# Kernel tuning notes

Hardware: AMD Instinct MI355X
Metric: run time of the kernel (lower is better)

## Reference

```python
import jax, jax.numpy as jnp
import numpy as np

D_STATE = 64
HEADDIM = 64
KD = 4

def _layernorm(x, w, b, eps=1e-5):
    m = jnp.mean(x, axis=-1, keepdims=True)
    v = jnp.mean((x - m) ** 2, axis=-1, keepdims=True)
    return (x - m) / jnp.sqrt(v + eps) * w + b

def _adaptive_pool_matrix(n_in, n_out):
    # torch AdaptiveAvgPool2d bin edges: [floor(i*n/o), ceil((i+1)*n/o))
    P = np.zeros((n_out, n_in), np.float32)
    for i in range(n_out):
        s = (i * n_in) // n_out
        e = -((-(i + 1) * n_in) // n_out)
        P[i, s:e] = 1.0 / (e - s)
    return jnp.asarray(P)

def _vss(x, i, vln_w, vln_b, vin_w, vin_b, vconv_w, vconv_b, vxproj_w, vdt_bias, vA_log, vD, von_w, von_b, vout_w, vout_b):
    # VSSBlock (m0_noz): x + SS2D(LayerNorm(x)); x: (Bt, H, W, C) channels-last
    xn = _layernorm(x, vln_w[i], vln_b[i])
    u = xn @ vin_w[i].T + vin_b[i]                      # (Bt,H,W,Din) in_proj (no z branch)
    Bt, H, W, Din = u.shape
    v = jnp.transpose(u, (0, 3, 1, 2))
    v = jax.lax.conv_general_dilated(v, vconv_w[i][:, None], (1, 1), [(1, 1), (1, 1)],
                                     feature_group_count=Din,
                                     dimension_numbers=('NCHW', 'OIHW', 'NCHW'))
    v = v + vconv_b[i][None, :, None, None]
    v = jax.nn.gelu(jnp.transpose(v, (0, 2, 3, 1)))     # depthwise 3x3 + act
    L = H * W
    NH = Din // HEADDIM
    x_row = v.reshape(Bt, L, Din)
    x_col = jnp.transpose(v, (0, 2, 1, 3)).reshape(Bt, L, Din)
    xs = jnp.stack([x_row, x_col, x_row[:, ::-1], x_col[:, ::-1]], 1)  # cross-scan (Bt,KD,L,Din)
    x_dbl = jnp.einsum('bkld,kcd->bklc', xs, vxproj_w[i])              # dt | B | C
    dts = jax.nn.softplus(x_dbl[..., :NH] + vdt_bias[i][None, :, None, :])  # (Bt,KD,L,NH)
    Bm = x_dbl[..., NH:NH + D_STATE]
    Cm = x_dbl[..., NH + D_STATE:]
    A = -jnp.exp(vA_log[i])                             # (KD,NH) scalar-per-head (mamba2)
    xh = xs.reshape(Bt, KD, L, NH, HEADDIM)
    def step(h, t):
        dt_t, x_t, B_t, C_t = t                         # (Bt,KD,NH),(Bt,KD,NH,hd),(Bt,KD,N),(Bt,KD,N)
        dA = jnp.exp(dt_t * A)
        h = h * dA[..., None, None] + (dt_t[..., None] * x_t)[..., None] * B_t[:, :, None, None, :]
        y = jnp.einsum('bkhdn,bkn->bkhd', h, C_t)
        return h, y
    h0 = jnp.zeros((Bt, KD, NH, HEADDIM, D_STATE), x.dtype)
    seq = (jnp.moveaxis(dts, 2, 0), jnp.moveaxis(xh, 2, 0), jnp.moveaxis(Bm, 2, 0), jnp.moveaxis(Cm, 2, 0))
    _, ys = jax.lax.scan(step, h0, seq)                 # (L,Bt,KD,NH,hd)
    ys = jnp.moveaxis(ys, 0, 2) + vD[i][None, :, None, :, None] * xh   # D skip per head
    ys = ys.reshape(Bt, KD, L, Din)
    def uncol(t):
        return jnp.transpose(t.reshape(Bt, W, H, Din), (0, 2, 1, 3)).reshape(Bt, L, Din)
    y = ys[:, 0] + uncol(ys[:, 1]) + ys[:, 2, ::-1] + uncol(ys[:, 3, ::-1])  # cross-merge
    y = _layernorm(y, von_w[i], von_b[i])
    out = y.reshape(Bt, H, W, Din) @ vout_w[i].T + vout_b[i]
    return x + out

def reference(style, mask, content, pos_embed_c, pos_embed_s, newps_w, newps_b,
              vln_w, vln_b, vin_w, vin_b, vconv_w, vconv_b, vxproj_w, vdt_bias, vA_log, vD,
              von_w, von_b, vout_w, vout_b, lin1_w, lin1_b, lin2_w, lin2_b,
              dn1_w, dn1_b, dn2_w, dn2_b, dn3_w, dn3_b, decnorm_w, decnorm_b):
    # mask and the incoming pos_embed_c are unused, matching the torch forward
    B, C, H, W = content.shape
    Ph = _adaptive_pool_matrix(H, 18)
    Pw = _adaptive_pool_matrix(W, 18)
    pooled = jnp.einsum('ih,bchw,jw->bcij', Ph, content, Pw)            # AdaptiveAvgPool2d(18)
    pos_c = jnp.einsum('oc,bcij->boij', newps_w, pooled) + newps_b[None, :, None, None]
    pos_c = jax.image.resize(pos_c, (B, C, style.shape[2], style.shape[3]), method='linear')
    def to_seq(t):  # (B,C,H,W) -> (HW, B, 1, C)
        return jnp.transpose(t.reshape(t.shape[0], t.shape[1], -1), (2, 0, 1))[:, :, None, :]
    s = to_seq(style); c = to_seq(content); ps = to_seq(pos_embed_s); pc = to_seq(pos_c)
    vss = lambda x, i: _vss(x, i, vln_w, vln_b, vin_w, vin_b, vconv_w, vconv_b, vxproj_w,
                            vdt_bias, vA_log, vD, von_w, von_b, vout_w, vout_b)
    s_enc = vss(s, 0)
    c_enc = vss(c, 1)
    q = c_enc + pc
    k = s_enc + ps
    tgt = _layernorm(c_enc + vss(q, 2), dn1_w, dn1_b)
    tgt = tgt + _layernorm(s_enc + vss(k, 3), dn2_w, dn2_b)
    ffn = jax.nn.gelu(tgt @ lin1_w.T + lin1_b) @ lin2_w.T + lin2_b
    tgt = _layernorm(tgt + ffn, dn3_w, dn3_b)
    tgt = _layernorm(tgt, decnorm_w, decnorm_b)
    hs = jnp.transpose(tgt[:, :, 0, :], (1, 2, 0))                      # (B,C,L)
    Hq = int(np.sqrt(hs.shape[-1]))
    return hs.reshape(B, C, -1, Hq)

def setup_inputs():
    key = jax.random.key(0)
    ks = jax.random.split(key, 16)
    D = 512; DIN = 512; NH = DIN // HEADDIM; NB = 4
    f = lambda k, shape, s=0.02: jax.random.normal(k, shape, jnp.float32) * s
    return {
        'style': jax.random.normal(ks[0], (4, 512, 16, 16), jnp.float32),
        'mask': jnp.zeros((4, 256), jnp.bool_),
        'content': jax.random.normal(ks[1], (4, 512, 16, 16), jnp.float32),
        'pos_embed_c': jax.random.normal(ks[2], (4, 512, 16, 16), jnp.float32),
        'pos_embed_s': jax.random.normal(ks[3], (4, 512, 16, 16), jnp.float32),
        'newps_w': f(ks[4], (512, 512)), 'newps_b': jnp.zeros((512,), jnp.float32),
        'vln_w': jnp.ones((NB, D), jnp.float32), 'vln_b': jnp.zeros((NB, D), jnp.float32),
        'vin_w': f(ks[5], (NB, DIN, D)), 'vin_b': jnp.zeros((NB, DIN), jnp.float32),
        'vconv_w': f(ks[6], (NB, DIN, 3, 3), 0.1), 'vconv_b': jnp.zeros((NB, DIN), jnp.float32),
        'vxproj_w': f(ks[7], (NB, KD, NH + 2 * D_STATE, DIN)),
        'vdt_bias': jnp.full((NB, KD, NH), -1.0, jnp.float32),
        'vA_log': f(ks[8], (NB, KD, NH), 0.1),
        'vD': jnp.ones((NB, KD, NH), jnp.float32),
        'von_w': jnp.ones((NB, DIN), jnp.float32), 'von_b': jnp.zeros((NB, DIN), jnp.float32),
        'vout_w': f(ks[9], (NB, D, DIN)), 'vout_b': jnp.zeros((NB, D), jnp.float32),
        'lin1_w': f(ks[10], (2048, D)), 'lin1_b': jnp.zeros((2048,), jnp.float32),
        'lin2_w': f(ks[11], (D, 2048)), 'lin2_b': jnp.zeros((D,), jnp.float32),
        'dn1_w': jnp.ones((D,), jnp.float32), 'dn1_b': jnp.zeros((D,), jnp.float32),
        'dn2_w': jnp.ones((D,), jnp.float32), 'dn2_b': jnp.zeros((D,), jnp.float32),
        'dn3_w': jnp.ones((D,), jnp.float32), 'dn3_b': jnp.zeros((D,), jnp.float32),
        'decnorm_w': jnp.ones((D,), jnp.float32), 'decnorm_b': jnp.zeros((D,), jnp.float32),
    }
```

## Files before the change

kernel.cpp:

```cpp
#include <hip/hip_runtime.h>
#include <hip/hip_bf16.h>
#include <math.h>

#define SEQ   524288
#define MROWS 1024
#define XDBL_P 557056

typedef __hip_bfloat16 bfloat;
typedef __bf16 bfx8 __attribute__((ext_vector_type(8)));
typedef float f32x4 __attribute__((ext_vector_type(4)));

__device__ __forceinline__ float gelu_tanh(float x){
    float x3 = x*x*x;
    float z = 0.7978845608028654f*(x + 0.044715f*x3);
    float az = fabsf(z);
    float e = __expf(-2.f*az);
    float th = copysignf((1.f - e)/(1.f + e), z);
    return 0.5f*x*(1.f + th);
}

__device__ __forceinline__ unsigned short bfbits(float x){
    union { __hip_bfloat16 h; unsigned short u; } cv;
    cv.h = __float2bfloat16(x);
    return cv.u;
}

__device__ __forceinline__ void glds16(const void* g, void* l){
    __builtin_amdgcn_global_load_lds(
        (const __attribute__((address_space(1))) unsigned int*)g,
        (__attribute__((address_space(3))) unsigned int*)l, 16, 0, 0);
}

#define VMWAIT(n) asm volatile("s_waitcnt vmcnt(" #n ")" ::: "memory")

__device__ __forceinline__ void ln_stats(const float* v, float& mean, float& rstd){
    float s = 0.f;
    #pragma unroll
    for (int t = 0; t < 8; ++t) s += v[t];
    #pragma unroll
    for (int off = 32; off > 0; off >>= 1) s += __shfl_xor(s, off, 64);
    mean = s * (1.f/512.f);
    float sq = 0.f;
    #pragma unroll
    for (int t = 0; t < 8; ++t){ float d = v[t] - mean; sq += d*d; }
    #pragma unroll
    for (int off = 32; off > 0; off >>= 1) sq += __shfl_xor(sq, off, 64);
    rstd = rsqrtf(sq * (1.f/512.f) + 1e-5f);
}

struct CvtArgs {
    const float* s[6];
    bfloat* d[6];
    int c4[6];
};
__global__ void prep_kernel(CvtArgs a,
                            const float* __restrict__ style,
                            const float* __restrict__ content,
                            const float* __restrict__ pos_s,
                            float* __restrict__ s_seq, float* __restrict__ c_seq,
                            float* __restrict__ ps_seq,
                            bfloat* __restrict__ pooledT)
{
    __shared__ float tsh[32][33];
    int blk = blockIdx.x;
    int tid = threadIdx.x;
    if (blk < 5440){
        int i = blk*256 + tid;
        int j = 0, base = 0;
        while (j < 5 && i >= a.c4[j]) { base = a.c4[j]; ++j; }
        int k = i - base;
        float4 v = ((const float4*)a.s[j])[k];
        union { bfloat h[4]; ushort4 u; } o;
        o.h[0] = __float2bfloat16(v.x); o.h[1] = __float2bfloat16(v.y);
        o.h[2] = __float2bfloat16(v.z); o.h[3] = __float2bfloat16(v.w);
        *(ushort4*)(a.d[j] + (size_t)k*4) = o.u;
    } else if (blk < 6976){
        int b2 = blk - 5440;
        int lt = b2 & 7;  b2 >>= 3;
        int ct = b2 & 15; b2 >>= 4;
        int b  = b2 & 3;  b2 >>= 2;
        const float* in = b2==0 ? style : (b2==1 ? content : pos_s);
        float* o = b2==0 ? s_seq : (b2==1 ? c_seq : ps_seq);
        int c0 = ct*32, l0 = lt*32;
        int lx = tid & 31, g = tid >> 5;
        #pragma unroll
        for (int qq = 0; qq < 4; ++qq){
            int cy = g + qq*8;
            tsh[cy][lx] = in[(size_t)(b*512 + c0+cy)*256 + l0 + lx];
        }
        __syncthreads();
        #pragma unroll
        for (int qq = 0; qq < 4; ++qq){
            int ly = g + qq*8;
            o[((size_t)(l0+ly)*4 + b)*512 + c0 + lx] = tsh[lx][ly];
        }
    } else {
        int bij = blk - 6976;
        int b = bij / 324;
        int ij = bij % 324;
        int i = ij / 18, jc = ij % 18;
        int s0 = (i*16)/18,  e0 = ((i+1)*16 + 17)/18;
        int s1 = (jc*16)/18, e1 = ((jc+1)*16 + 17)/18;
        float inv = 1.0f / (float)((e0-s0)*(e1-s1));
        for (int c = tid; c < 512; c += 256){
            float acc = 0.f;
            for (int h = s0; h < e0; ++h)
                for (int w = s1; w < e1; ++w)
                    acc += content[((b*512 + c)*16 + h)*16 + w];
            pooledT[(size_t)(b*324 + ij)*512 + c] = __float2bfloat16(acc * inv);
        }
    }
}

__device__ __forceinline__ int resize_taps(int o, float* w, int* j0_out){
    const float inv_scale = 18.0f/16.0f;
    float sf = (o + 0.5f)*inv_scale - 0.5f;
    int j0 = (int)ceilf(sf - inv_scale);
    int j1 = (int)floorf(sf + inv_scale);
    if (j0 < 0) j0 = 0;
    if (j1 > 17) j1 = 17;
    int n = j1 - j0 + 1;
    float sum = 0.f;
    for (int t = 0; t < n; ++t){
        float d = fabsf(sf - (float)(j0 + t)) * (16.0f/18.0f);
        float v = fmaxf(0.f, 1.f - d);
        w[t] = v; sum += v;
    }
    float r = 1.f / sum;
    for (int t = 0; t < n; ++t) w[t] *= r;
    *j0_out = j0;
    return n;
}

__global__ void resize_kernel(const float* __restrict__ pc18T, float* __restrict__ pc_seq){
    int bid = blockIdx.x;
    int b = bid >> 8;
    int yx = bid & 255;
    int y = yx >> 4, x = yx & 15;
    float wy[3], wx[3];
    int jy0, jx0;
    int ny = resize_taps(y, wy, &jy0);
    int nx = resize_taps(x, wx, &jx0);
    for (int c = threadIdx.x; c < 512; c += 256){
        float acc = 0.f;
        for (int ty = 0; ty < ny; ++ty)
            for (int tx = 0; tx < nx; ++tx)
                acc += wy[ty]*wx[tx] *
                       pc18T[(size_t)(b*324 + (jy0+ty)*18 + (jx0+tx))*512 + c];
        pc_seq[(size_t)((y*16 + x)*4 + b)*512 + c] = acc;
    }
}

__global__ __launch_bounds__(256) void ln_vss_pair_kernel(
    const float* __restrict__ x0, const float* __restrict__ x20,
    const float* __restrict__ x1, const float* __restrict__ x21,
    const float* __restrict__ wall, const float* __restrict__ ball,
    int ibase, bfloat* __restrict__ outb)
{
    int row = blockIdx.x*4 + (threadIdx.x >> 6);
    int lane = threadIdx.x & 63;
    int p = row >> 10, r2 = row & 1023;
    const float* in0 = (p ? x1 : x0) + (size_t)r2*512;
    const float* in1 = p ? x21 : x20;
    const float* w = wall + (ibase+p)*512;
    const float* b = ball + (ibase+p)*512;
    int base = lane*8;
    float v[8];
    #pragma unroll
    for (int t = 0; t < 8; ++t){
        v[t] = in0[base + t];
        if (in1) v[t] += in1[(size_t)r2*512 + base + t];
    }
    float mean, rstd;
    ln_stats(v, mean, rstd);
    bfloat* o = outb + (size_t)p*SEQ + (size_t)r2*512 + base;
    union { ushort u[8]; uint4 q; } pk;
    #pragma unroll
    for (int t = 0; t < 8; ++t)
        pk.u[t] = bfbits((v[t] - mean)*rstd*w[base + t] + b[base + t]);
    *(uint4*)o = pk.q;
}

__global__ __launch_bounds__(256) void dn_pair_kernel(
    const float* __restrict__ a0, const float* __restrict__ a1,
    const float* __restrict__ w1, const float* __restrict__ b1,
    const float* __restrict__ c0, const float* __restrict__ c1,
    const float* __restrict__ w2, const float* __restrict__ b2,
    float* __restrict__ outf, bfloat* __restrict__ outb)
{
    int row = blockIdx.x*4 + (threadIdx.x >> 6);
    int lane = threadIdx.x & 63;
    int base = lane*8;
    size_t ro = (size_t)row*512 + base;
    float va[8], vc[8];
    #pragma unroll
    for (int t = 0; t < 8; ++t){ va[t] = a0[ro+t] + a1[ro+t]; vc[t] = c0[ro+t] + c1[ro+t]; }
    float m1, r1, m2, r2;
    ln_stats(va, m1, r1);
    ln_stats(vc, m2, r2);
    union { ushort u[8]; uint4 q; } pk;
    #pragma unroll
    for (int t = 0; t < 8; ++t){
        float o = (va[t]-m1)*r1*w1[base+t] + b1[base+t]
                + (vc[t]-m2)*r2*w2[base+t] + b2[base+t];
        outf[ro + t] = o;
        pk.u[t] = bfbits(o);
    }
    *(uint4*)(outb + ro) = pk.q;
}

__global__ __launch_bounds__(256) void ln2_out_kernel(
    const float* __restrict__ in0, const float* __restrict__ in1,
    const float* __restrict__ w1, const float* __restrict__ b1,
    const float* __restrict__ w2, const float* __restrict__ b2,
    float* __restrict__ out)
{
    int row = blockIdx.x*4 + (threadIdx.x >> 6);
    int lane = threadIdx.x & 63;
    int base = lane*8;
    size_t ro = (size_t)row*512 + base;
    float v[8];
    #pragma unroll
    for (int t = 0; t < 8; ++t) v[t] = in0[ro+t] + in1[ro+t];
    float mean, rstd;
    ln_stats(v, mean, rstd);
    #pragma unroll
    for (int t = 0; t < 8; ++t) v[t] = (v[t]-mean)*rstd*w1[base+t] + b1[base+t];
    ln_stats(v, mean, rstd);
    int l = row >> 2, b = row & 3;
    #pragma unroll
    for (int t = 0; t < 8; ++t){
        float o = (v[t]-mean)*rstd*w2[base+t] + b2[base+t];
        out[(size_t)(b*512 + base + t)*256 + l] = o;
    }
}

struct GJob {
    const bfloat* A; const bfloat* W;
    const float* bias; const float* res1; const float* res2;
    float* Cf; bfloat* Cb;
    const float* cw; const float* cb;
    bfloat* vb;
    int arev;
};

__global__ __launch_bounds__(256) void gemm3_kernel(
    GJob J0, GJob J1, GJob J2, GJob J3,
    int M, int N, int K, int nbn, int epi)
{
    __shared__ __align__(16) char lds[65536];
    const int z = blockIdx.z;
    GJob j = (z==0) ? J0 : (z==1) ? J1 : (z==2) ? J2 : J3;

    int nwg = gridDim.x;
    int orig = blockIdx.x;
    int q = nwg >> 3, r = nwg & 7;
    int xcd = orig & 7, off = orig >> 3;
    int wgid = (xcd < r ? xcd*(q+1) : r*(q+1) + (xcd-r)*q) + off;
    int bm = (wgid / nbn) * 64;
    int bn = (wgid % nbn) * 64;

    const int tid = threadIdx.x;
    const int wv = tid >> 6, ln = tid & 63;

    const int r0 = tid >> 3;
    const int cs = (tid & 7) ^ (r0 & 7);
    int ar0 = bm + r0;       if (ar0 > M-1) ar0 = M-1;
    int ar1 = bm + r0 + 32;  if (ar1 > M-1) ar1 = M-1;
    if (j.arev){ ar0 = (ar0 & ~3) | (3 - (ar0 & 3)); ar1 = (ar1 & ~3) | (3 - (ar1 & 3)); }
    int br0 = bn + r0;       if (br0 > N-1) br0 = N-1;
    int br1 = bn + r0 + 32;  if (br1 > N-1) br1 = N-1;
    const bfloat* a0p = j.A + (size_t)ar0*K + cs*8;
    const bfloat* a1p = j.A + (size_t)ar1*K + cs*8;
    const bfloat* b0p = j.W + (size_t)br0*K + cs*8;
    const bfloat* b1p = j.W + (size_t)br1*K + cs*8;

    auto STAGE = [&](int bb, int k0){
        char* base = lds + bb*16384 + wv*1024;
        glds16(a0p + k0, base);
        glds16(a1p + k0, base + 4096);
        glds16(b0p + k0, base + 8192);
        glds16(b1p + k0, base + 12288);
    };

    const int wr = wv >> 1, wc = wv & 1;
    const int fr = ln & 15, fc = ln >> 4;
    f32x4 acc[2][2] = {};

    auto COMP = [&](int bb){
        char* bA = lds + bb*16384;
        char* bB = bA + 8192;
        int ra0 = wr*32 + fr, ra1 = ra0 + 16;
        int rb0 = wc*32 + fr, rb1 = rb0 + 16;
        #pragma unroll
        for (int kk = 0; kk < 2; ++kk){
            int ch = kk*4 + fc;
            bfx8 a0 = *(const bfx8*)(bA + ra0*128 + ((ch ^ (ra0&7))<<4));
            bfx8 a1 = *(const bfx8*)(bA + ra1*128 + ((ch ^ (ra1&7))<<4));
            bfx8 b0 = *(const bfx8*)(bB + rb0*128 + ((ch ^ (rb0&7))<<4));
            bfx8 b1 = *(const bfx8*)(bB + rb1*128 + ((ch ^ (rb1&7))<<4));
            acc[0][0] = __builtin_amdgcn_mfma_f32_16x16x32_bf16(a0,b0,acc[0][0],0,0,0);
            acc[0][1] = __builtin_amdgcn_mfma_f32_16x16x32_bf16(a0,b1,acc[0][1],0,0,0);
            acc[1][0] = __builtin_amdgcn_mfma_f32_16x16x32_bf16(a1,b0,acc[1][0],0,0,0);
            acc[1][1] = __builtin_amdgcn_mfma_f32_16x16x32_bf16(a1,b1,acc[1][1],0,0,0);
        }
    };

    const int nt = K >> 6;
    for (int s = 0; s < 3 && s < nt; ++s) STAGE(s, s << 6);
    for (int t = 0; t < nt; ++t){
        int rem = nt - 1 - t;
        if (rem >= 2)      VMWAIT(8);
        else if (rem == 1) VMWAIT(4);
        else               VMWAIT(0);
        __builtin_amdgcn_sched_barrier(0);
        __builtin_amdgcn_s_barrier();
        if (t + 3 < nt) STAGE((t+3) & 3, (t+3) << 6);
        COMP(t & 3);
    }

    const int er = (ln >> 4) * 4;
    const int ec = ln & 15;

    if (epi == 2){
        __syncthreads();
        float* ut = (float*)lds;
        #pragma unroll
        for (int i = 0; i < 2; ++i)
        #pragma unroll
        for (int jj = 0; jj < 2; ++jj)
        #pragma unroll
        for (int rr = 0; rr < 4; ++rr){
            int ml = wr*32 + i*16 + er + rr;
            int nl = wc*32 + jj*16 + ec;
            ut[ml*65 + nl] = acc[i][jj][rr] + j.bias[bn + nl];
        }
        __syncthreads();
        int rrow = tid >> 2, c0 = (tid & 3) * 16;
        int bt4 = rrow & ~3, lv = rrow & 3;
        int m = bm + rrow;
        float g[16];
        #pragma unroll
        for (int c = 0; c < 16; ++c){
            int n = bn + c0 + c;
            float a = j.cb[n];
            #pragma unroll
            for (int kh = 0; kh < 3; ++kh){
                int hh = lv + kh - 1;
                if (hh >= 0 && hh < 4)
                    a += ut[(bt4 + hh)*65 + c0 + c] * j.cw[(n*3 + kh)*3 + 1];
            }
            g[c] = gelu_tanh(a);
        }
        union { ushort u[8]; uint4 qv; } pk;
        #pragma unroll
        for (int h = 0; h < 2; ++h){
            #pragma unroll
            for (int t = 0; t < 8; ++t) pk.u[t] = bfbits(g[h*8 + t]);
            *(uint4*)(j.vb + (size_t)m*512 + bn + c0 + h*8) = pk.qv;
        }
        return;
    }

    #pragma unroll
    for (int i = 0; i < 2; ++i)
    #pragma unroll
    for (int jj = 0; jj < 2; ++jj)
    #pragma unroll
    for (int rr = 0; rr < 4; ++rr){
        int m = bm + wr*32 + i*16 + er + rr;
        int n = bn + wc*32 + jj*16 + ec;
        if (m >= M || n >= N) continue;
        float v = acc[i][jj][rr];
        if (j.bias) v += j.bias[n];
        if (epi == 1) v = gelu_tanh(v);
        if (j.res1) v += j.res1[(size_t)m*N + n];
        if (j.res2) v += j.res2[(size_t)m*N + n];
        if (epi == 3){
            int k2 = n >= 136;
            int cc = n - (k2 ? 136 : 0);
            j.Cf[((size_t)(k2*1024 + m))*136 + cc] = v;
        } else {
            if (j.Cf) j.Cf[(size_t)m*N + n] = v;
            if (j.Cb) j.Cb[(size_t)m*N + n] = __float2bfloat16(v);
        }
    }
}

__global__ __launch_bounds__(256) void scan_fused_kernel(
    const float* __restrict__ xdbl,
    const bfloat* __restrict__ vb,
    const float* __restrict__ dt_bias,
    const float* __restrict__ A_log,
    const float* __restrict__ Dp,
    const float* __restrict__ von_w, const float* __restrict__ von_b,
    int ibase, bfloat* __restrict__ outb)
{
    __shared__ float yb[4][4][512];
    int blk = blockIdx.x;
    int p = blk >> 8, bt = blk & 255;
    int k = threadIdx.x >> 6, lane = threadIdx.x & 63;

    const float* xd = xdbl + (size_t)p*XDBL_P + (size_t)(k*1024 + bt*4)*136;

    float bb[4], cc[4];
    #pragma unroll
    for (int l = 0; l < 4; ++l){
        bb[l] = xd[l*136 + 8 + lane];
        cc[l] = xd[l*136 + 72 + lane];
    }

    int sl = (lane & 31) >> 3, snh = lane & 7;
    float Aval = -expf(A_log[p*32 + k*8 + snh]);
    float draw = xd[sl*136 + snh] + dt_bias[p*32 + k*8 + snh];
    float dtv = fmaxf(draw, 0.f) + log1pf(expf(-fabsf(draw)));
    float dAv = expf(dtv * Aval);

    float s[16];
    #pragma unroll
    for (int l = 0; l < 4; ++l)
    #pragma unroll
    for (int jj = 0; jj < 4; ++jj)
        s[l*4+jj] = cc[l]*bb[jj];
    #pragma unroll
    for (int off = 32; off > 0; off >>= 1)
        #pragma unroll
        for (int i = 0; i < 16; ++i)
            s[i] += __shfl_xor(s[i], off, 64);

    float x[4][8];
    #pragma unroll
    for (int lp = 0; lp < 4; ++lp){
        int row = bt*4 + ((k < 2) ? lp : 3 - lp);
        const bfloat* xr = vb + (size_t)p*SEQ + (size_t)row*512 + lane;
        #pragma unroll
        for (int nh = 0; nh < 8; ++nh) x[lp][nh] = __bfloat162float(xr[nh*64]);
    }

    #pragma unroll
    for (int nh = 0; nh < 8; ++nh){
        float dtl[4], dal[4];
        #pragma unroll
        for (int l = 0; l < 4; ++l){
            dtl[l] = __shfl(dtv, l*8 + nh, 64);
            dal[l] = __shfl(dAv, l*8 + nh, 64);
        }
        float Dv = Dp[p*32 + k*8 + nh];
        float coef[4] = {0.f, 0.f, 0.f, 0.f};
        #pragma unroll
        for (int l = 0; l < 4; ++l){
            #pragma unroll
            for (int jj = 0; jj < 4; ++jj) coef[jj] *= dal[l];
            coef[l] = dtl[l];
            float y = Dv * x[l][nh];
            #pragma unroll
            for (int jj = 0; jj <= l; ++jj) y += coef[jj]*s[l*4+jj]*x[jj][nh];
            yb[k][l][nh*64 + lane] = y;
        }
    }
    __syncthreads();

    int l = k, rl = 3 - k;
    int base = lane*8;
    float vv[8];
    #pragma unroll
    for (int t = 0; t < 8; ++t)
        vv[t] = yb[0][l][base+t] + yb[1][l][base+t]
              + yb[2][rl][base+t] + yb[3][rl][base+t];
    float mean, rstd;
    ln_stats(vv, mean, rstd);
    const float* w = von_w + (ibase+p)*512;
    const float* bv = von_b + (ibase+p)*512;
    union { ushort u[8]; uint4 qv; } pk;
    #pragma unroll
    for (int t = 0; t < 8; ++t)
        pk.u[t] = bfbits((vv[t]-mean)*rstd*w[base+t] + bv[base+t]);
    *(uint4*)(outb + (size_t)p*SEQ + (size_t)(bt*4 + l)*512 + base) = pk.qv;
}

extern "C" void kernel_launch(void* const* d_in, const int* in_sizes, int n_in,
                              void* d_out, int out_size, void* d_ws, size_t ws_size,
                              hipStream_t stream)
{
    const float* style   = (const float*)d_in[0];
    const float* content = (const float*)d_in[2];
    const float* pos_s   = (const float*)d_in[4];
    const float* newps_w = (const float*)d_in[5];
    const float* newps_b = (const float*)d_in[6];
    const float* vln_w   = (const float*)d_in[7];
    const float* vln_b   = (const float*)d_in[8];
    const float* vin_b   = (const float*)d_in[10];
    const float* vconv_w = (const float*)d_in[11];
    const float* vconv_b = (const float*)d_in[12];
    const float* vdt_bias= (const float*)d_in[14];
    const float* vA_log  = (const float*)d_in[15];
    const float* vD      = (const float*)d_in[16];
    const float* von_w   = (const float*)d_in[17];
    const float* von_b   = (const float*)d_in[18];
    const float* vout_b  = (const float*)d_in[20];
    const float* lin1_b  = (const float*)d_in[22];
    const float* lin2_b  = (const float*)d_in[24];
    const float* dn1_w   = (const float*)d_in[25];
    const float* dn1_b   = (const float*)d_in[26];
    const float* dn2_w   = (const float*)d_in[27];
    const float* dn2_b   = (const float*)d_in[28];
    const float* dn3_w   = (const float*)d_in[29];
    const float* dn3_b   = (const float*)d_in[30];
    const float* decn_w  = (const float*)d_in[31];
    const float* decn_b  = (const float*)d_in[32];

    float* out = (float*)d_out;
    float* ws  = (float*)d_ws;

    float* s_seq  = ws + (size_t) 0*SEQ;
    float* c_seq  = ws + (size_t) 1*SEQ;
    float* ps_seq = ws + (size_t) 2*SEQ;
    float* pc_seq = ws + (size_t) 3*SEQ;
    float* s_enc  = ws + (size_t) 4*SEQ;
    float* c_enc  = ws + (size_t) 5*SEQ;
    float* t1     = ws + (size_t) 6*SEQ;
    float* t2     = ws + (size_t) 7*SEQ;
    float* tgt    = ws + (size_t) 8*SEQ;
    float* ffnout = ws + (size_t) 9*SEQ;
    float* xdbl   = ws + (size_t)10*SEQ;
    float* pc18T  = ws + (size_t)13*SEQ;

    bfloat* wb = (bfloat*)(ws + (size_t)15*SEQ);
    bfloat* wb_vin    = wb;
    bfloat* wb_xproj  = wb + 1048576;
    bfloat* wb_vout   = wb + 2162688;
    bfloat* wb_lin1   = wb + 3211264;
    bfloat* wb_lin2   = wb + 4259840;
    bfloat* wb_newps  = wb + 5308416;
    bfloat* xn_bf     = wb + 5570560;
    bfloat* vbuf_bf   = xn_bf   + (size_t)2*SEQ;
    bfloat* tgt_bf    = vbuf_bf + (size_t)2*SEQ;
    bfloat* ffn_bf    = tgt_bf  + (size_t)SEQ;
    bfloat* pooled_bf = ffn_bf;

    auto launch_gemm = [&](GJob* jobs, int nz, int M, int N, int K, int epi){
        int nbm = (M + 63)/64, nbn = (N + 63)/64;
        dim3 g(nbm*nbn, 1, nz);
        gemm3_kernel<<<g, 256, 0, stream>>>(jobs[0], jobs[nz>1?1:0],
                                            jobs[nz>2?2:0], jobs[nz>3?3:0],
                                            M, N, K, nbn, epi);
    };

    GJob Z = {};

    auto vss_pair = [&](const float* xa, const float* x2a,
                        const float* xb, const float* x2b,
                        int ibase, float* oa, float* ob){
        ln_vss_pair_kernel<<<512, 256, 0, stream>>>(xa, x2a, xb, x2b,
                                                    vln_w, vln_b, ibase, xn_bf);
        GJob jv[2];
        for (int p = 0; p < 2; ++p){
            int i = ibase + p;
            jv[p] = Z;
            jv[p].A = xn_bf + (size_t)p*SEQ;
            jv[p].W = wb_vin + (size_t)i*262144;
            jv[p].bias = vin_b + i*512;
            jv[p].cw = vconv_w + (size_t)i*4608;
            jv[p].cb = vconv_b + i*512;
            jv[p].vb = vbuf_bf + (size_t)p*SEQ;
        }
        launch_gemm(jv, 2, MROWS, 512, 512, 2);

        GJob jx[4];
        for (int zz = 0; zz < 4; ++zz){
            int p = zz >> 1, rev = zz & 1, i = ibase + p;
            jx[zz] = Z;
            jx[zz].A = vbuf_bf + (size_t)p*SEQ;
            jx[zz].arev = rev;
            jx[zz].W = wb_xproj + (size_t)i*278528 + (size_t)rev*272*512;
            jx[zz].Cf = xdbl + (size_t)p*XDBL_P + (size_t)rev*278528;
        }
        launch_gemm(jx, 4, MROWS, 272, 512, 3);

        scan_fused_kernel<<<512, 256, 0, stream>>>(xdbl, vbuf_bf,
                                                   vdt_bias + ibase*32,
                                                   vA_log + ibase*32,
                                                   vD + ibase*32,
                                                   von_w, von_b, ibase, xn_bf);

        GJob jo[2];
        const float* r1[2] = {xa, xb};
        const float* r2[2] = {x2a, x2b};
        float* oo[2] = {oa, ob};
        for (int p = 0; p < 2; ++p){
            int i = ibase + p;
            jo[p] = Z;
            jo[p].A = xn_bf + (size_t)p*SEQ;
            jo[p].W = wb_vout + (size_t)i*262144;
            jo[p].bias = vout_b + i*512;
            jo[p].res1 = r1[p];
            jo[p].res2 = r2[p];
            jo[p].Cf = oo[p];
        }
        launch_gemm(jo, 2, MROWS, 512, 512, 0);
    };

    CvtArgs ca;
    ca.s[0]=(const float*)d_in[9];  ca.d[0]=wb_vin;
    ca.s[1]=(const float*)d_in[13]; ca.d[1]=wb_xproj;
    ca.s[2]=(const float*)d_in[19]; ca.d[2]=wb_vout;
    ca.s[3]=(const float*)d_in[21]; ca.d[3]=wb_lin1;
    ca.s[4]=(const float*)d_in[23]; ca.d[4]=wb_lin2;
    ca.s[5]=newps_w;                ca.d[5]=wb_newps;
    ca.c4[0]=262144; ca.c4[1]=540672; ca.c4[2]=802816;
    ca.c4[3]=1064960; ca.c4[4]=1327104; ca.c4[5]=1392640;
    prep_kernel<<<8272, 256, 0, stream>>>(ca, style, content, pos_s,
                                          s_seq, c_seq, ps_seq, pooled_bf);

    GJob jn = Z;
    jn.A = pooled_bf; jn.W = wb_newps; jn.bias = newps_b; jn.Cf = pc18T;
    launch_gemm(&jn, 1, 1296, 512, 512, 0);
    resize_kernel<<<1024, 256, 0, stream>>>(pc18T, pc_seq);

    vss_pair(s_seq, nullptr, c_seq, nullptr, 0, s_enc, c_enc);

    vss_pair(c_enc, pc_seq, s_enc, ps_seq, 2, t1, t2);
    dn_pair_kernel<<<256, 256, 0, stream>>>(c_enc, t1, dn1_w, dn1_b,
                                            s_enc, t2, dn2_w, dn2_b,
                                            tgt, tgt_bf);

    GJob jf = Z;
    jf.A = tgt_bf; jf.W = wb_lin1; jf.bias = lin1_b; jf.Cb = ffn_bf;
    launch_gemm(&jf, 1, MROWS, 2048, 512, 1);
    GJob jg = Z;
    jg.A = ffn_bf; jg.W = wb_lin2; jg.bias = lin2_b; jg.Cf = ffnout;
    launch_gemm(&jg, 1, MROWS, 512, 2048, 0);
    ln2_out_kernel<<<256, 256, 0, stream>>>(tgt, ffnout, dn3_w, dn3_b,
                                            decn_w, decn_b, out);
}
```

Baseline: 166.1 us.

## Fuse first LayerNorm into prep and batch heterogeneous GEMM jobs per launch

```diff
diff --git a/kernel.cpp b/kernel.cpp
--- a/kernel.cpp
+++ b/kernel.cpp
@@ -46,70 +46,6 @@
     #pragma unroll
     for (int off = 32; off > 0; off >>= 1) sq += __shfl_xor(sq, off, 64);
     rstd = rsqrtf(sq * (1.f/512.f) + 1e-5f);
-}
-
-struct CvtArgs {
-    const float* s[6];
-    bfloat* d[6];
-    int c4[6];
-};
-__global__ void prep_kernel(CvtArgs a,
-                            const float* __restrict__ style,
-                            const float* __restrict__ content,
-                            const float* __restrict__ pos_s,
-                            float* __restrict__ s_seq, float* __restrict__ c_seq,
-                            float* __restrict__ ps_seq,
-                            bfloat* __restrict__ pooledT)
-{
-    __shared__ float tsh[32][33];
-    int blk = blockIdx.x;
-    int tid = threadIdx.x;
-    if (blk < 5440){
-        int i = blk*256 + tid;
-        int j = 0, base = 0;
-        while (j < 5 && i >= a.c4[j]) { base = a.c4[j]; ++j; }
-        int k = i - base;
-        float4 v = ((const float4*)a.s[j])[k];
-        union { bfloat h[4]; ushort4 u; } o;
-        o.h[0] = __float2bfloat16(v.x); o.h[1] = __float2bfloat16(v.y);
-        o.h[2] = __float2bfloat16(v.z); o.h[3] = __float2bfloat16(v.w);
-        *(ushort4*)(a.d[j] + (size_t)k*4) = o.u;
-    } else if (blk < 6976){
-        int b2 = blk - 5440;
-        int lt = b2 & 7;  b2 >>= 3;
-        int ct = b2 & 15; b2 >>= 4;
-        int b  = b2 & 3;  b2 >>= 2;
-        const float* in = b2==0 ? style : (b2==1 ? content : pos_s);
-        float* o = b2==0 ? s_seq : (b2==1 ? c_seq : ps_seq);
-        int c0 = ct*32, l0 = lt*32;
-        int lx = tid & 31, g = tid >> 5;
-        #pragma unroll
-        for (int qq = 0; qq < 4; ++qq){
-            int cy = g + qq*8;
-            tsh[cy][lx] = in[(size_t)(b*512 + c0+cy)*256 + l0 + lx];
-        }
-        __syncthreads();
-        #pragma unroll
-        for (int qq = 0; qq < 4; ++qq){
-            int ly = g + qq*8;
-            o[((size_t)(l0+ly)*4 + b)*512 + c0 + lx] = tsh[lx][ly];
-        }
-    } else {
-        int bij = blk - 6976;
-        int b = bij / 324;
-        int ij = bij % 324;
-        int i = ij / 18, jc = ij % 18;
-        int s0 = (i*16)/18,  e0 = ((i+1)*16 + 17)/18;
-        int s1 = (jc*16)/18, e1 = ((jc+1)*16 + 17)/18;
-        float inv = 1.0f / (float)((e0-s0)*(e1-s1));
-        for (int c = tid; c < 512; c += 256){
-            float acc = 0.f;
-            for (int h = s0; h < e0; ++h)
-                for (int w = s1; w < e1; ++w)
-                    acc += content[((b*512 + c)*16 + h)*16 + w];
-            pooledT[(size_t)(b*324 + ij)*512 + c] = __float2bfloat16(acc * inv);
-        }
-    }
 }
 
 __device__ __forceinline__ int resize_taps(int o, float* w, int* j0_out){
@@ -132,22 +68,105 @@
     return n;
 }
 
-__global__ void resize_kernel(const float* __restrict__ pc18T, float* __restrict__ pc_seq){
-    int bid = blockIdx.x;
-    int b = bid >> 8;
-    int yx = bid & 255;
-    int y = yx >> 4, x = yx & 15;
-    float wy[3], wx[3];
-    int jy0, jx0;
-    int ny = resize_taps(y, wy, &jy0);
-    int nx = resize_taps(x, wx, &jx0);
-    for (int c = threadIdx.x; c < 512; c += 256){
-        float acc = 0.f;
-        for (int ty = 0; ty < ny; ++ty)
-            for (int tx = 0; tx < nx; ++tx)
-                acc += wy[ty]*wx[tx] *
-                       pc18T[(size_t)(b*324 + (jy0+ty)*18 + (jx0+tx))*512 + c];
-        pc_seq[(size_t)((y*16 + x)*4 + b)*512 + c] = acc;
+struct CvtArgs {
+    const float* s[6];
+    bfloat* d[6];
+    int c4[6];
+};
+__global__ __launch_bounds__(256) void prep_kernel(CvtArgs a,
+                            const float* __restrict__ style,
+                            const float* __restrict__ content,
+                            const float* __restrict__ pos_s,
+                            float* __restrict__ s_seq, float* __restrict__ c_seq,
+                            float* __restrict__ ps_seq,
+                            const float* __restrict__ vln_w,
+                            const float* __restrict__ vln_b,
+                            bfloat* __restrict__ xn_bf,
+                            bfloat* __restrict__ pooledT)
+{
+    __shared__ float tsh[32][33];
+    __shared__ float trow[8][513];
+    int blk = blockIdx.x;
+    int tid = threadIdx.x;
+    if (blk < 5440){
+        int i = blk*256 + tid;
+        int j = 0, base = 0;
+        while (j < 5 && i >= a.c4[j]) { base = a.c4[j]; ++j; }
+        int k = i - base;
+        float4 v = ((const float4*)a.s[j])[k];
+        union { bfloat h[4]; ushort4 u; } o;
+        o.h[0] = __float2bfloat16(v.x); o.h[1] = __float2bfloat16(v.y);
+        o.h[2] = __float2bfloat16(v.z); o.h[3] = __float2bfloat16(v.w);
+        *(ushort4*)(a.d[j] + (size_t)k*4) = o.u;
+    } else if (blk < 5952){
+        int b2 = blk - 5440;
+        int lt = b2 & 7;  b2 >>= 3;
+        int ct = b2 & 15; b2 >>= 4;
+        int b  = b2 & 3;
+        int c0 = ct*32, l0 = lt*32;
+        int lx = tid & 31, g = tid >> 5;
+        #pragma unroll
+        for (int qq = 0; qq < 4; ++qq){
+            int cy = g + qq*8;
+            tsh[cy][lx] = pos_s[(size_t)(b*512 + c0+cy)*256 + l0 + lx];
+        }
+        __syncthreads();
+        #pragma unroll
+        for (int qq = 0; qq < 4; ++qq){
+            int ly = g + qq*8;
+            ps_seq[((size_t)(l0+ly)*4 + b)*512 + c0 + lx] = tsh[lx][ly];
+        }
+    } else if (blk < 6208){
+        int b3 = blk - 5952;
+        int lt = b3 & 31;  int b = (b3 >> 5) & 3;  int p = b3 >> 7;
+        const float* in = p ? content : style;
+        float* oseq = p ? c_seq : s_seq;
+        int l0 = lt*8;
+        #pragma unroll
+        for (int h = 0; h < 2; ++h){
+            int c = tid*2 + h;
+            const float* src = in + (size_t)(b*512 + c)*256 + l0;
+            float4 f0 = *(const float4*)(src);
+            float4 f1 = *(const float4*)(src + 4);
+            trow[0][c] = f0.x; trow[1][c] = f0.y; trow[2][c] = f0.z; trow[3][c] = f0.w;
+            trow[4][c] = f1.x; trow[5][c] = f1.y; trow[6][c] = f1.z; trow[7][c] = f1.w;
+        }
+        __syncthreads();
+        int wv = tid >> 6, lane = tid & 63, base = lane*8;
+        const float* w = vln_w + p*512;
+        const float* bb = vln_b + p*512;
+        #pragma unroll
+        for (int rr = 0; rr < 2; ++rr){
+            int dl = wv*2 + rr;
+            int row = (l0 + dl)*4 + b;
+            float v[8];
+            #pragma unroll
+            for (int t = 0; t < 8; ++t) v[t] = trow[dl][base + t];
+            *(float4*)(oseq + (size_t)row*512 + base)     = make_float4(v[0],v[1],v[2],v[3]);
+            *(float4*)(oseq + (size_t)row*512 + base + 4) = make_float4(v[4],v[5],v[6],v[7]);
+            float mean, rstd;
+            ln_stats(v, mean, rstd);
+            union { ushort u[8]; uint4 q; } pk;
+            #pragma unroll
+            for (int t = 0; t < 8; ++t)
+                pk.u[t] = bfbits((v[t]-mean)*rstd*w[base+t] + bb[base+t]);
+            *(uint4*)(xn_bf + (size_t)p*SEQ + (size_t)row*512 + base) = pk.q;
+        }
+    } else {
+        int bij = blk - 6208;
+        int b = bij / 324;
+        int ij = bij % 324;
+        int i = ij / 18, jc = ij % 18;
+        int s0 = (i*16)/18,  e0 = ((i+1)*16 + 17)/18;
+        int s1 = (jc*16)/18, e1 = ((jc+1)*16 + 17)/18;
+        float inv = 1.0f / (float)((e0-s0)*(e1-s1));
+        for (int c = tid; c < 512; c += 256){
+            float acc = 0.f;
+            for (int h = s0; h < e0; ++h)
+                for (int w = s1; w < e1; ++w)
+                    acc += content[((b*512 + c)*16 + h)*16 + w];
+            pooledT[(size_t)(b*324 + ij)*512 + c] = __float2bfloat16(acc * inv);
+        }
     }
 }
 
@@ -241,28 +260,52 @@
     float* Cf; bfloat* Cb;
     const float* cw; const float* cb;
     bfloat* vb;
-    int arev;
+    int arev, M, N, K, nbn, nblk, epi;
 };
-
-__global__ __launch_bounds__(256) void gemm3_kernel(
-    GJob J0, GJob J1, GJob J2, GJob J3,
-    int M, int N, int K, int nbn, int epi)
+struct GBatch { GJob j[5]; int cum[5]; int nj; };
+
+__global__ __launch_bounds__(256) void gemm_multi_kernel(GBatch B)
 {
     __shared__ __align__(16) char lds[65536];
-    const int z = blockIdx.z;
-    GJob j = (z==0) ? J0 : (z==1) ? J1 : (z==2) ? J2 : J3;
-
-    int nwg = gridDim.x;
-    int orig = blockIdx.x;
+    int bi = blockIdx.x;
+    int ji = 0, start = 0;
+    while (ji < B.nj - 1 && bi >= B.cum[ji]){ start = B.cum[ji]; ++ji; }
+    GJob j = B.j[ji];
+    int wgid0 = bi - start;
+    const int tid = threadIdx.x;
+
+    if (j.epi == 4){
+        #pragma unroll
+        for (int qq = 0; qq < 16; ++qq){
+            int pos = wgid0*16 + qq;
+            int b = pos >> 8;
+            int y = (pos >> 4) & 15, x = pos & 15;
+            float wy[3], wx[3];
+            int jy0, jx0;
+            int ny = resize_taps(y, wy, &jy0);
+            int nx = resize_taps(x, wx, &jx0);
+            const float* src = j.res1;
+            for (int c = tid; c < 512; c += 256){
+                float acc = 0.f;
+                for (int ty = 0; ty < ny; ++ty)
+                    for (int tx = 0; tx < nx; ++tx)
+                        acc += wy[ty]*wx[tx] *
+                               src[(size_t)(b*324 + (jy0+ty)*18 + (jx0+tx))*512 + c];
+                j.Cf[(size_t)((y*16 + x)*4 + b)*512 + c] = acc;
+            }
+        }
+        return;
+    }
+
+    const int M = j.M, N = j.N, K = j.K, nbn = j.nbn;
+    int nwg = j.nblk;
     int q = nwg >> 3, r = nwg & 7;
-    int xcd = orig & 7, off = orig >> 3;
+    int xcd = wgid0 & 7, off = wgid0 >> 3;
     int wgid = (xcd < r ? xcd*(q+1) : r*(q+1) + (xcd-r)*q) + off;
     int bm = (wgid / nbn) * 64;
     int bn = (wgid % nbn) * 64;
 
-    const int tid = threadIdx.x;
     const int wv = tid >> 6, ln = tid & 63;
-
     const int r0 = tid >> 3;
     const int cs = (tid & 7) ^ (r0 & 7);
     int ar0 = bm + r0;       if (ar0 > M-1) ar0 = M-1;
@@ -322,7 +365,7 @@
     const int er = (ln >> 4) * 4;
     const int ec = ln & 15;
 
-    if (epi == 2){
+    if (j.epi == 2){
         __syncthreads();
         float* ut = (float*)lds;
         #pragma unroll
@@ -373,10 +416,10 @@
         if (m >= M || n >= N) continue;
         float v = acc[i][jj][rr];
         if (j.bias) v += j.bias[n];
-        if (epi == 1) v = gelu_tanh(v);
+        if (j.epi == 1) v = gelu_tanh(v);
         if (j.res1) v += j.res1[(size_t)m*N + n];
         if (j.res2) v += j.res2[(size_t)m*N + n];
-        if (epi == 3){
+        if (j.epi == 3){
             int k2 = n >= 136;
             int cc = n - (k2 ? 136 : 0);
             j.Cf[((size_t)(k2*1024 + m))*136 + cc] = v;
@@ -538,66 +581,29 @@
     bfloat* ffn_bf    = tgt_bf  + (size_t)SEQ;
     bfloat* pooled_bf = ffn_bf;
 
-    auto launch_gemm = [&](GJob* jobs, int nz, int M, int N, int K, int epi){
-        int nbm = (M + 63)/64, nbn = (N + 63)/64;
-        dim3 g(nbm*nbn, 1, nz);
-        gemm3_kernel<<<g, 256, 0, stream>>>(jobs[0], jobs[nz>1?1:0],
-                                            jobs[nz>2?2:0], jobs[nz>3?3:0],
-                                            M, N, K, nbn, epi);
+    GJob Z = {};
+
+    auto mk = [&](const bfloat* A, const bfloat* W, const float* bias,
+                  const float* r1, const float* r2, float* Cf, bfloat* Cb,
+                  int M, int N, int K, int epi, int arev)->GJob{
+        GJob g = Z;
+        g.A = A; g.W = W; g.bias = bias; g.res1 = r1; g.res2 = r2;
+        g.Cf = Cf; g.Cb = Cb; g.M = M; g.N = N; g.K = K;
+        g.nbn = (N + 63)/64; g.nblk = ((M + 63)/64) * g.nbn;
+        g.epi = epi; g.arev = arev;
+        return g;
     };
 
-    GJob Z = {};
-
-    auto vss_pair = [&](const float* xa, const float* x2a,
-                        const float* xb, const float* x2b,
-                        int ibase, float* oa, float* ob){
-        ln_vss_pair_kernel<<<512, 256, 0, stream>>>(xa, x2a, xb, x2b,
-                                                    vln_w, vln_b, ibase, xn_bf);
-        GJob jv[2];
-        for (int p = 0; p < 2; ++p){
-            int i = ibase + p;
-            jv[p] = Z;
-            jv[p].A = xn_bf + (size_t)p*SEQ;
-            jv[p].W = wb_vin + (size_t)i*262144;
-            jv[p].bias = vin_b + i*512;
-            jv[p].cw = vconv_w + (size_t)i*4608;
-            jv[p].cb = vconv_b + i*512;
-            jv[p].vb = vbuf_bf + (size_t)p*SEQ;
-        }
-        launch_gemm(jv, 2, MROWS, 512, 512, 2);
-
-        GJob jx[4];
-        for (int zz = 0; zz < 4; ++zz){
-            int p = zz >> 1, rev = zz & 1, i = ibase + p;
-            jx[zz] = Z;
-            jx[zz].A = vbuf_bf + (size_t)p*SEQ;
-            jx[zz].arev = rev;
-            jx[zz].W = wb_xproj + (size_t)i*278528 + (size_t)rev*272*512;
-            jx[zz].Cf = xdbl + (size_t)p*XDBL_P + (size_t)rev*278528;
-        }
-        launch_gemm(jx, 4, MROWS, 272, 512, 3);
-
-        scan_fused_kernel<<<512, 256, 0, stream>>>(xdbl, vbuf_bf,
-                                                   vdt_bias + ibase*32,
-                                                   vA_log + ibase*32,
-                                                   vD + ibase*32,
-                                                   von_w, von_b, ibase, xn_bf);
-
-        GJob jo[2];
-        const float* r1[2] = {xa, xb};
-        const float* r2[2] = {x2a, x2b};
-        float* oo[2] = {oa, ob};
-        for (int p = 0; p < 2; ++p){
-            int i = ibase + p;
-            jo[p] = Z;
-            jo[p].A = xn_bf + (size_t)p*SEQ;
-            jo[p].W = wb_vout + (size_t)i*262144;
-            jo[p].bias = vout_b + i*512;
-            jo[p].res1 = r1[p];
-            jo[p].res2 = r2[p];
-            jo[p].Cf = oo[p];
-        }
-        launch_gemm(jo, 2, MROWS, 512, 512, 0);
+    auto launch_multi = [&](GJob* jobs, int nj){
+        GBatch B;
+        int cum = 0;
+        for (int i = 0; i < nj; ++i){
+            B.j[i] = jobs[i];
+            cum += jobs[i].nblk;
+            B.cum[i] = cum;
+        }
+        B.nj = nj;
+        gemm_multi_kernel<<<cum, 256, 0, stream>>>(B);
     };
 
     CvtArgs ca;
@@ -609,27 +615,84 @@
     ca.s[5]=newps_w;                ca.d[5]=wb_newps;
     ca.c4[0]=262144; ca.c4[1]=540672; ca.c4[2]=802816;
     ca.c4[3]=1064960; ca.c4[4]=1327104; ca.c4[5]=1392640;
-    prep_kernel<<<8272, 256, 0, stream>>>(ca, style, content, pos_s,
-                                          s_seq, c_seq, ps_seq, pooled_bf);
-
-    GJob jn = Z;
-    jn.A = pooled_bf; jn.W = wb_newps; jn.bias = newps_b; jn.Cf = pc18T;
-    launch_gemm(&jn, 1, 1296, 512, 512, 0);
-    resize_kernel<<<1024, 256, 0, stream>>>(pc18T, pc_seq);
-
-    vss_pair(s_seq, nullptr, c_seq, nullptr, 0, s_enc, c_enc);
-
-    vss_pair(c_enc, pc_seq, s_enc, ps_seq, 2, t1, t2);
+    prep_kernel<<<7504, 256, 0, stream>>>(ca, style, content, pos_s,
+                                          s_seq, c_seq, ps_seq,
+                                          vln_w, vln_b, xn_bf, pooled_bf);
+
+    auto vss_mid_tail = [&](int ibase, const float* xa, const float* x2a,
+                            const float* xb, const float* x2b,
+                            float* oa, float* ob, int enc){
+        GJob jv[3];
+        for (int p = 0; p < 2; ++p){
+            int i = ibase + p;
+            jv[p] = mk(xn_bf + (size_t)p*SEQ, wb_vin + (size_t)i*262144,
+                       vin_b + i*512, nullptr, nullptr, nullptr, nullptr,
+                       MROWS, 512, 512, 2, 0);
+            jv[p].cw = vconv_w + (size_t)i*4608;
+            jv[p].cb = vconv_b + i*512;
+            jv[p].vb = vbuf_bf + (size_t)p*SEQ;
+        }
+        int nvj = 2;
+        if (enc){
+            jv[2] = mk(pooled_bf, wb_newps, newps_b, nullptr, nullptr,
+                       pc18T, nullptr, 1296, 512, 512, 0, 0);
+            nvj = 3;
+        }
+        launch_multi(jv, nvj);
+
+        GJob jx[5];
+        for (int zz = 0; zz < 4; ++zz){
+            int p = zz >> 1, rev = zz & 1, i = ibase + p;
+            jx[zz] = mk(vbuf_bf + (size_t)p*SEQ,
+                        wb_xproj + (size_t)i*278528 + (size_t)rev*272*512,
+                        nullptr, nullptr, nullptr,
+                        xdbl + (size_t)p*XDBL_P + (size_t)rev*278528, nullptr,
+                        MROWS, 272, 512, 3, rev);
+        }
+        int nxj = 4;
+        if (enc){
+            jx[4] = Z;
+            jx[4].epi = 4; jx[4].nblk = 64;
+            jx[4].res1 = pc18T; jx[4].Cf = pc_seq;
+            nxj = 5;
+        }
+        launch_multi(jx, nxj);
+
+        scan_fused_kernel<<<512, 256, 0, stream>>>(xdbl, vbuf_bf,
+                                                   vdt_bias + ibase*32,
+                                                   vA_log + ibase*32,
+                                                   vD + ibase*32,
+                                                   von_w, von_b, ibase, xn_bf);
+
+        GJob jo[2];
+        const float* r1[2] = {xa, xb};
+        const float* r2[2] = {x2a, x2b};
+        float* oo[2] = {oa, ob};
+        for (int p = 0; p < 2; ++p){
+            int i = ibase + p;
+            jo[p] = mk(xn_bf + (size_t)p*SEQ, wb_vout + (size_t)i*262144,
+                       vout_b + i*512, r1[p], r2[p], oo[p], nullptr,
+                       MROWS, 512, 512, 0, 0);
+        }
+        launch_multi(jo, 2);
+    };
+
+    vss_mid_tail(0, s_seq, nullptr, c_seq, nullptr, s_enc, c_enc, 1);
+
+    ln_vss_pair_kernel<<<512, 256, 0, stream>>>(c_enc, pc_seq, s_enc, ps_seq,
+                                                vln_w, vln_b, 2, xn_bf);
+    vss_mid_tail(2, c_enc, pc_seq, s_enc, ps_seq, t1, t2, 0);
+
     dn_pair_kernel<<<256, 256, 0, stream>>>(c_enc, t1, dn1_w, dn1_b,
                                             s_enc, t2, dn2_w, dn2_b,
                                             tgt, tgt_bf);
 
-    GJob jf = Z;
-    jf.A = tgt_bf; jf.W = wb_lin1; jf.bias = lin1_b; jf.Cb = ffn_bf;
-    launch_gemm(&jf, 1, MROWS, 2048, 512, 1);
-    GJob jg = Z;
-    jg.A = ffn_bf; jg.W = wb_lin2; jg.bias = lin2_b; jg.Cf = ffnout;
-    launch_gemm(&jg, 1, MROWS, 512, 2048, 0);
+    GJob jf = mk(tgt_bf, wb_lin1, lin1_b, nullptr, nullptr,
+                 nullptr, ffn_bf, MROWS, 2048, 512, 1, 0);
+    launch_multi(&jf, 1);
+    GJob jg = mk(ffn_bf, wb_lin2, lin2_b, nullptr, nullptr,
+                 ffnout, nullptr, MROWS, 512, 2048, 0, 0);
+    launch_multi(&jg, 1);
     ln2_out_kernel<<<256, 256, 0, stream>>>(tgt, ffnout, dn3_w, dn3_b,
                                             decn_w, decn_b, out);
 }
```

New measurement: 177.0 us. 1.07x slower.
